# Optimization experiments

Measured on AMD Instinct MI355X. Metric: run time of the kernel, lower is better.

## Reference

```python
import jax, jax.numpy as jnp
import numpy as np

N = 50000
NEG_SLOPE = 0.2


def add_self_loops(edge_index, n):
    loops = jnp.arange(n, dtype=edge_index.dtype)
    return jnp.concatenate([edge_index, jnp.stack([loops, loops])], axis=1)


def gat_layer(x, edge_index, W, a_src, a_dst, b, heads, ch):
    # x: [N, F_in], W: [F_in, heads*ch], a_src/a_dst: [heads, ch], b: [heads*ch]
    n = x.shape[0]
    src, dst = edge_index[0], edge_index[1]
    h = (x @ W).reshape(n, heads, ch)                      # [N, H, C]
    alpha_src = jnp.sum(h * a_src, axis=-1)                # [N, H]
    alpha_dst = jnp.sum(h * a_dst, axis=-1)                # [N, H]
    e = jax.nn.leaky_relu(alpha_src[src] + alpha_dst[dst], NEG_SLOPE)  # [E, H]
    # segment softmax over incoming edges of each destination node
    m = jax.ops.segment_max(e, dst, num_segments=n)        # [N, H]
    ex = jnp.exp(e - m[dst])                               # [E, H]
    denom = jax.ops.segment_sum(ex, dst, num_segments=n)   # [N, H]
    alpha = ex / (denom[dst] + 1e-16)                      # [E, H]
    msg = h[src] * alpha[:, :, None]                       # [E, H, C]
    out = jax.ops.segment_sum(msg, dst, num_segments=n)    # [N, H, C]
    return out.reshape(n, heads * ch) + b


def setup_inputs() -> dict:
    key = jax.random.key(0)
    ks = jax.random.split(key, 12)
    input_dim, hidden_dim, output_dim, heads = 128, 32, 64, 4
    E = 1600000
    x = jax.random.normal(ks[0], (N, input_dim), dtype=jnp.float32)
    edge_index = jax.random.randint(ks[1], (2, E), 0, N, dtype=jnp.int64)
    s1 = 1.0 / np.sqrt(input_dim)
    s2 = 1.0 / np.sqrt(hidden_dim * heads)
    W1 = jax.random.uniform(ks[2], (input_dim, heads * hidden_dim), jnp.float32, -s1, s1)
    a_src1 = jax.random.uniform(ks[3], (heads, hidden_dim), jnp.float32, -s1, s1)
    a_dst1 = jax.random.uniform(ks[4], (heads, hidden_dim), jnp.float32, -s1, s1)
    b1 = jnp.zeros((heads * hidden_dim,), jnp.float32)
    W2 = jax.random.uniform(ks[5], (heads * hidden_dim, output_dim), jnp.float32, -s2, s2)
    a_src2 = jax.random.uniform(ks[6], (1, output_dim), jnp.float32, -s2, s2)
    a_dst2 = jax.random.uniform(ks[7], (1, output_dim), jnp.float32, -s2, s2)
    b2 = jnp.zeros((output_dim,), jnp.float32)
    return {"x": x, "edge_index": edge_index,
            "W1": W1, "a_src1": a_src1, "a_dst1": a_dst1, "b1": b1,
            "W2": W2, "a_src2": a_src2, "a_dst2": a_dst2, "b2": b2}


def reference(x, edge_index, W1, a_src1, a_dst1, b1, W2, a_src2, a_dst2, b2):
    n = x.shape[0]
    ei = add_self_loops(edge_index, n)
    h = gat_layer(x, ei, W1, a_src1, a_dst1, b1, heads=4, ch=32)
    h = jax.nn.relu(h)
    out = gat_layer(h, ei, W2, a_src2, a_dst2, b2, heads=1, ch=64)
    return out
```

## Files before the change

### kernel.cpp

```cpp
#include <hip/hip_runtime.h>
#include <hip/hip_bf16.h>
#include <hip/hip_fp16.h>


#define LRELU_SLOPE 0.2f
#define NBMAX 200
#define NBLK  512
#define BCAP  16384
#define CAPIMG 16384

typedef _Float16 f16x8 __attribute__((ext_vector_type(8)));
typedef float f32x4 __attribute__((ext_vector_type(4)));


__global__ __launch_bounds__(256) void hist_kernel(const int* __restrict__ ei_dst,
                                                   int* __restrict__ hist, int E, int chunk) {
    __shared__ int h[NBMAX];
    int t = threadIdx.x;
    for (int i = t; i < NBMAX; i += 256) h[i] = 0;
    __syncthreads();
    int begin = blockIdx.x * chunk;
    int endE = min(E, begin + chunk);
    for (int e = begin + t; e < endE; e += 256) atomicAdd(&h[ei_dst[e] >> 8], 1);
    __syncthreads();
    for (int i = t; i < NBMAX; i += 256) hist[i * NBLK + blockIdx.x] = h[i];
}

__global__ __launch_bounds__(512) void bucket_scan_kernel(int* __restrict__ hist,
                                                          int* __restrict__ gfill) {
    __shared__ int buf[2][NBLK];
    int b = blockIdx.x, t = threadIdx.x;
    buf[0][t] = hist[b * NBLK + t];
    __syncthreads();
    int pi = 0;
#pragma unroll
    for (int off = 1; off < NBLK; off <<= 1) {
        int v = buf[pi][t];
        if (t >= off) v += buf[pi][t - off];
        buf[pi ^ 1][t] = v;
        __syncthreads();
        pi ^= 1;
    }
    hist[b * NBLK + t] = (t == 0) ? 0 : buf[pi][t - 1];
    if (t == 0) gfill[b] = buf[pi][NBLK - 1];
}

__global__ __launch_bounds__(256) void scatter2_kernel(const int* __restrict__ ei_src,
                                                       const int* __restrict__ ei_dst,
                                                       const int* __restrict__ hist,
                                                       unsigned int* __restrict__ records,
                                                       int E, int chunk) {
    __shared__ int base[NBMAX];
    __shared__ int lcnt[NBMAX];
    int t = threadIdx.x;
    for (int i = t; i < NBMAX; i += 256) {
        base[i] = hist[i * NBLK + blockIdx.x];
        lcnt[i] = 0;
    }
    __syncthreads();
    int begin = blockIdx.x * chunk;
    int endE = min(E, begin + chunk);
    for (int e = begin + t; e < endE; e += 256) {
        int s = ei_src[e], d = ei_dst[e];
        int bkt = d >> 8;
        unsigned int rec = (unsigned int)d | ((unsigned int)s << 16);
        int r = atomicAdd(&lcnt[bkt], 1);
        records[(size_t)bkt * BCAP + base[bkt] + r] = rec;
    }
}

__global__ __launch_bounds__(256) void deg_kernel(const unsigned int* __restrict__ records,
                                                  const int* __restrict__ gfill,
                                                  int* __restrict__ deg, int N) {
    __shared__ int cnt[256];
    int t = threadIdx.x, b = blockIdx.x;
    cnt[t] = 1;
    __syncthreads();
    int c = gfill[b];
    const unsigned int* r = records + (size_t)b * BCAP;
    for (int i = t; i < c; i += 256) atomicAdd(&cnt[r[i] & 255], 1);
    __syncthreads();
    int gi = (b << 8) + t;
    if (gi < N) deg[gi] = cnt[t];
}

__global__ __launch_bounds__(256) void scan_blocksums_kernel(const int* __restrict__ gfill,
                                                             int* __restrict__ bsums,
                                                             int* __restrict__ row_ptr,
                                                             int nblocks, int n, int total) {
    __shared__ int buf[2][256];
    int t = threadIdx.x;
    int v0 = 0;
    if (t < nblocks) v0 = gfill[t] + min(256, n - (t << 8));
    buf[0][t] = v0;
    __syncthreads();
    int pi = 0;
#pragma unroll
    for (int off = 1; off < 256; off <<= 1) {
        int v = buf[pi][t];
        if (t >= off) v += buf[pi][t - off];
        buf[pi ^ 1][t] = v;
        __syncthreads();
        pi ^= 1;
    }
    if (t < nblocks) bsums[t] = (t == 0) ? 0 : buf[pi][t - 1];
    if (t == 0) row_ptr[n] = total;
}

__global__ __launch_bounds__(256) void scan_down_kernel(const int* __restrict__ deg,
                                                        const int* __restrict__ blockSums,
                                                        int* __restrict__ row_ptr, int n) {
    __shared__ int buf[2][256];
    int t = threadIdx.x;
    int i = blockIdx.x * 256 + t;
    int d = (i < n) ? deg[i] : 0;
    buf[0][t] = d;
    __syncthreads();
    int pi = 0;
#pragma unroll
    for (int off = 1; off < 256; off <<= 1) {
        int v = buf[pi][t];
        if (t >= off) v += buf[pi][t - off];
        buf[pi ^ 1][t] = v;
        __syncthreads();
        pi ^= 1;
    }
    if (i < n) row_ptr[i] = blockSums[blockIdx.x] + buf[pi][t] - d;
}

__global__ __launch_bounds__(256) void csr_scatter_kernel(const unsigned int* __restrict__ records,
                                                          const int* __restrict__ gfill,
                                                          const int* __restrict__ row_ptr,
                                                          unsigned short* __restrict__ col,
                                                          int N) {
    __shared__ unsigned short img[CAPIMG];
    __shared__ int lfill[256];
    int t = threadIdx.x, b = blockIdx.x;
    int bBase = b << 8;
    int bEnd = min(bBase + 256, N);
    int rbase = row_ptr[bBase];
    int size = row_ptr[bEnd] - rbase;
    bool lds = (size <= CAPIMG);
    int gi = bBase + t;
    if (gi < bEnd) {
        int rp = row_ptr[gi];
        int local = rp - rbase;
        lfill[t] = local + 1;
        if (lds) img[local] = (unsigned short)gi;
        else col[rp] = (unsigned short)gi;
    }
    __syncthreads();
    int c = gfill[b];
    const unsigned int* r = records + (size_t)b * BCAP;
    for (int i = t; i < c; i += 256) {
        unsigned int rec = r[i];
        int d8 = rec & 255;
        unsigned short s = (unsigned short)(rec >> 16);
        int p = atomicAdd(&lfill[d8], 1);
        if (lds) img[p] = s;
        else col[rbase + p] = s;
    }
    __syncthreads();
    if (lds) {
        for (int i = t; i < size; i += 256) col[rbase + i] = img[i];
    }
}


__global__ __launch_bounds__(256) void gemm1_mfma_kernel(const float* __restrict__ X,
                                                         const float* __restrict__ W,
                                                         __half* __restrict__ outh,
                                                         const float* __restrict__ a_src,
                                                         const float* __restrict__ a_dst,
                                                         float* __restrict__ as_out,
                                                         float* __restrict__ ad_out, int nrows) {
    constexpr int KP = 136;
    __shared__ _Float16 wlds[128 * KP];
    int t = threadIdx.x;
    int wv = t >> 6, lane = t & 63;
    int quad = lane >> 4, m16 = lane & 15;
    for (int i = t; i < 4096; i += 256) {
        int k = i >> 5;
        int n0 = (i & 31) << 2;
        float4 v = *(const float4*)(W + k * 128 + n0);
        wlds[(n0 + 0) * KP + k] = (_Float16)v.x;
        wlds[(n0 + 1) * KP + k] = (_Float16)v.y;
        wlds[(n0 + 2) * KP + k] = (_Float16)v.z;
        wlds[(n0 + 3) * KP + k] = (_Float16)v.w;
    }
    __syncthreads();

    int row = blockIdx.x * 64 + wv * 16 + m16;
    int rowC = min(row, nrows - 1);
    const float* xp = X + (size_t)rowC * 128;

    f32x4 acc[8];
#pragma unroll
    for (int nt = 0; nt < 8; ++nt) acc[nt] = (f32x4)0.f;

    for (int kt = 0; kt < 128; kt += 32) {
        float4 v0 = *(const float4*)(xp + kt + quad * 8);
        float4 v1 = *(const float4*)(xp + kt + quad * 8 + 4);
        f16x8 af;
        af[0] = (_Float16)v0.x; af[1] = (_Float16)v0.y;
        af[2] = (_Float16)v0.z; af[3] = (_Float16)v0.w;
        af[4] = (_Float16)v1.x; af[5] = (_Float16)v1.y;
        af[6] = (_Float16)v1.z; af[7] = (_Float16)v1.w;
#pragma unroll
        for (int nt = 0; nt < 8; ++nt) {
            f16x8 bf = *(const f16x8*)(&wlds[(nt * 16 + m16) * KP + kt + quad * 8]);
            acc[nt] = __builtin_amdgcn_mfma_f32_16x16x32_f16(af, bf, acc[nt], 0, 0, 0);
        }
    }

    float aS[8], aD[8];
#pragma unroll
    for (int nt = 0; nt < 8; ++nt) {
        aS[nt] = a_src[nt * 16 + m16];
        aD[nt] = a_dst[nt * 16 + m16];
    }
    int rowBaseW = blockIdx.x * 64 + wv * 16;
#pragma unroll
    for (int r = 0; r < 4; ++r) {
        int orow = rowBaseW + quad * 4 + r;
        bool ov = orow < nrows;
        if (ov) {
#pragma unroll
            for (int nt = 0; nt < 8; ++nt)
                outh[(size_t)orow * 128 + nt * 16 + m16] = __float2half(acc[nt][r]);
        }
#pragma unroll
        for (int h = 0; h < 4; ++h) {
            float ss = acc[2 * h][r] * aS[2 * h] + acc[2 * h + 1][r] * aS[2 * h + 1];
            float dd = acc[2 * h][r] * aD[2 * h] + acc[2 * h + 1][r] * aD[2 * h + 1];
#pragma unroll
            for (int o = 1; o < 16; o <<= 1) {
                ss += __shfl_xor(ss, o, 64);
                dd += __shfl_xor(dd, o, 64);
            }
            if (ov && m16 == h) {
                as_out[orow * 4 + h] = ss;
                ad_out[orow * 4 + h] = dd;
            }
        }
    }
}


__global__ __launch_bounds__(256) void gemm2_mfma_kernel(const __half* __restrict__ Xh,
                                                         const float* __restrict__ W,
                                                         __half* __restrict__ outh,
                                                         const float* __restrict__ a_src,
                                                         const float* __restrict__ a_dst,
                                                         float* __restrict__ as_out,
                                                         float* __restrict__ ad_out, int nrows) {
    constexpr int KP = 136;
    __shared__ _Float16 wlds[64 * KP];
    int t = threadIdx.x;
    int wv = t >> 6, lane = t & 63;
    int quad = lane >> 4, m16 = lane & 15;
    for (int i = t; i < 2048; i += 256) {
        int k = i >> 4;
        int n0 = (i & 15) << 2;
        float4 v = *(const float4*)(W + k * 64 + n0);
        wlds[(n0 + 0) * KP + k] = (_Float16)v.x;
        wlds[(n0 + 1) * KP + k] = (_Float16)v.y;
        wlds[(n0 + 2) * KP + k] = (_Float16)v.z;
        wlds[(n0 + 3) * KP + k] = (_Float16)v.w;
    }
    __syncthreads();

    int row = blockIdx.x * 64 + wv * 16 + m16;
    int rowC = min(row, nrows - 1);
    const _Float16* xp = (const _Float16*)Xh + (size_t)rowC * 128;

    f32x4 acc[4];
#pragma unroll
    for (int nt = 0; nt < 4; ++nt) acc[nt] = (f32x4)0.f;

    for (int kt = 0; kt < 128; kt += 32) {
        f16x8 af = *(const f16x8*)(xp + kt + quad * 8);
#pragma unroll
        for (int nt = 0; nt < 4; ++nt) {
            f16x8 bf = *(const f16x8*)(&wlds[(nt * 16 + m16) * KP + kt + quad * 8]);
            acc[nt] = __builtin_amdgcn_mfma_f32_16x16x32_f16(af, bf, acc[nt], 0, 0, 0);
        }
    }

    float aS[4], aD[4];
#pragma unroll
    for (int nt = 0; nt < 4; ++nt) {
        aS[nt] = a_src[nt * 16 + m16];
        aD[nt] = a_dst[nt * 16 + m16];
    }
    int rowBaseW = blockIdx.x * 64 + wv * 16;
#pragma unroll
    for (int r = 0; r < 4; ++r) {
        int orow = rowBaseW + quad * 4 + r;
        bool ov = orow < nrows;
        if (ov) {
#pragma unroll
            for (int nt = 0; nt < 4; ++nt)
                outh[(size_t)orow * 64 + nt * 16 + m16] = __float2half(acc[nt][r]);
        }
        float ss = 0.f, dd = 0.f;
#pragma unroll
        for (int nt = 0; nt < 4; ++nt) {
            ss = fmaf(acc[nt][r], aS[nt], ss);
            dd = fmaf(acc[nt][r], aD[nt], dd);
        }
#pragma unroll
        for (int o = 1; o < 16; o <<= 1) {
            ss += __shfl_xor(ss, o, 64);
            dd += __shfl_xor(dd, o, 64);
        }
        if (ov && m16 == 0) {
            as_out[orow] = ss;
            ad_out[orow] = dd;
        }
    }
}


__global__ __launch_bounds__(256) void agg1_kernel(const __half2* __restrict__ h1h,
                                                   const float* __restrict__ asrc,
                                                   const float* __restrict__ adst,
                                                   const int* __restrict__ row_ptr,
                                                   const unsigned short* __restrict__ col,
                                                   const float* __restrict__ b1,
                                                   __half2* __restrict__ out, int n) {
    int wave = threadIdx.x >> 6;
    int lane = threadIdx.x & 63;
    int node = blockIdx.x * 4 + wave;
    if (node >= n) return;
    int head = lane >> 4;
    int hp1 = lane & 3;
    int j16 = lane >> 2;
    float ad1 = adst[node * 4 + hp1];
    int start = row_ptr[node], end = row_ptr[node + 1];
    float accx = 0.f, accy = 0.f, s = 0.f;
    for (int base = start; base < end; base += 64) {
        int idx = base + lane;
        int cnt = min(64, end - base);
        int myS = (idx < end) ? (int)col[idx] : 0;
        float pr[4];
#pragma unroll
        for (int e = 0; e < 4; ++e) {
            int j = e * 16 + j16;
            int srcj = __shfl(myS, j, 64);
            float ev = asrc[srcj * 4 + hp1] + ad1;
            ev = (ev > 0.f) ? ev : LRELU_SLOPE * ev;
            pr[e] = (j < cnt) ? __expf(ev) : 0.f;
        }
#pragma unroll
        for (int e = 0; e < 4; ++e) {
            int ebase = e << 4;
            if (ebase < cnt) {
                float pre = pr[e];
                int rem4 = min(16, ((cnt - ebase) + 3) & ~3);
                for (int jj = 0; jj < rem4; jj += 4) {
                    int j0 = ebase + jj;
                    unsigned s0 = (unsigned)__shfl(myS, j0, 64);
                    unsigned s1 = (unsigned)__shfl(myS, j0 + 1, 64);
                    unsigned s2 = (unsigned)__shfl(myS, j0 + 2, 64);
                    unsigned s3 = (unsigned)__shfl(myS, j0 + 3, 64);
                    float p0 = __shfl(pre, (jj + 0) * 4 + head, 64);
                    float p1 = __shfl(pre, (jj + 1) * 4 + head, 64);
                    float p2 = __shfl(pre, (jj + 2) * 4 + head, 64);
                    float p3 = __shfl(pre, (jj + 3) * 4 + head, 64);
                    float2 f0 = __half22float2(h1h[(s0 << 6) | lane]);
                    float2 f1 = __half22float2(h1h[(s1 << 6) | lane]);
                    float2 f2 = __half22float2(h1h[(s2 << 6) | lane]);
                    float2 f3 = __half22float2(h1h[(s3 << 6) | lane]);
                    accx = fmaf(p0, f0.x, accx);
                    accy = fmaf(p0, f0.y, accy);
                    accx = fmaf(p1, f1.x, accx);
                    accy = fmaf(p1, f1.y, accy);
                    accx = fmaf(p2, f2.x, accx);
                    accy = fmaf(p2, f2.y, accy);
                    accx = fmaf(p3, f3.x, accx);
                    accy = fmaf(p3, f3.y, accy);
                    s += (p0 + p1) + (p2 + p3);
                }
            }
        }
    }
    float inv = 1.f / (s + 1e-16f);
    float2 bb = ((const float2*)b1)[lane];
    float ox = fmaxf(accx * inv + bb.x, 0.f);
    float oy = fmaxf(accy * inv + bb.y, 0.f);
    out[((unsigned)node << 6) | lane] = __floats2half2_rn(ox, oy);
}

__global__ __launch_bounds__(256) void agg2_kernel(const __half2* __restrict__ h2bh,
                                                   const float* __restrict__ asrc,
                                                   const float* __restrict__ adst,
                                                   const int* __restrict__ row_ptr,
                                                   const unsigned short* __restrict__ col,
                                                   const float* __restrict__ b2,
                                                   float* __restrict__ out, int n) {
    int wave = threadIdx.x >> 6;
    int lane = threadIdx.x & 63;
    int node = blockIdx.x * 4 + wave;
    if (node >= n) return;
    int half = lane >> 5;
    int m = lane & 31;
    float ad = adst[node];
    int start = row_ptr[node], end = row_ptr[node + 1];
    float accx = 0.f, accy = 0.f, s = 0.f;
    for (int base = start; base < end; base += 64) {
        int idx = base + lane;
        int cnt = min(64, end - base);
        int myS = (idx < end) ? (int)col[idx] : 0;
        float ev = asrc[myS] + ad;
        ev = (ev > 0.f) ? ev : LRELU_SLOPE * ev;
        float pr = (lane < cnt) ? __expf(ev) : 0.f;
        for (int j = 0; j < cnt; j += 8) {
            int j0 = j + half;
            unsigned s0 = (unsigned)__shfl(myS, j0, 64);
            unsigned s1 = (unsigned)__shfl(myS, j0 + 2, 64);
            unsigned s2 = (unsigned)__shfl(myS, j0 + 4, 64);
            unsigned s3 = (unsigned)__shfl(myS, j0 + 6, 64);
            float p0 = __shfl(pr, j0, 64);
            float p1 = __shfl(pr, j0 + 2, 64);
            float p2 = __shfl(pr, j0 + 4, 64);
            float p3 = __shfl(pr, j0 + 6, 64);
            float2 f0 = __half22float2(h2bh[(s0 << 5) | m]);
            float2 f1 = __half22float2(h2bh[(s1 << 5) | m]);
            float2 f2 = __half22float2(h2bh[(s2 << 5) | m]);
            float2 f3 = __half22float2(h2bh[(s3 << 5) | m]);
            accx = fmaf(p0, f0.x, accx);
            accy = fmaf(p0, f0.y, accy);
            accx = fmaf(p1, f1.x, accx);
            accy = fmaf(p1, f1.y, accy);
            accx = fmaf(p2, f2.x, accx);
            accy = fmaf(p2, f2.y, accy);
            accx = fmaf(p3, f3.x, accx);
            accy = fmaf(p3, f3.y, accy);
            s += (p0 + p1) + (p2 + p3);
        }
    }
    s += __shfl_xor(s, 32, 64);
    accx += __shfl_xor(accx, 32, 64);
    accy += __shfl_xor(accy, 32, 64);
    if (half == 0) {
        float inv = 1.f / (s + 1e-16f);
        float2 bb = ((const float2*)b2)[m];
        float2 o;
        o.x = accx * inv + bb.x;
        o.y = accy * inv + bb.y;
        *(float2*)(out + (size_t)node * 64 + 2 * m) = o;
    }
}


extern "C" void kernel_launch(void* const* d_in, const int* in_sizes, int n_in,
                              void* d_out, int out_size, void* d_ws, size_t ws_size,
                              hipStream_t stream) {
    const float* x      = (const float*)d_in[0];
    const int*   ei     = (const int*)d_in[1];
    const float* W1     = (const float*)d_in[2];
    const float* a_src1 = (const float*)d_in[3];
    const float* a_dst1 = (const float*)d_in[4];
    const float* b1     = (const float*)d_in[5];
    const float* W2     = (const float*)d_in[6];
    const float* a_src2 = (const float*)d_in[7];
    const float* a_dst2 = (const float*)d_in[8];
    const float* b2     = (const float*)d_in[9];
    float* out = (float*)d_out;

    const int N = in_sizes[0] / 128;
    const int E = in_sizes[1] / 2;
    const int total = E + N;
    const int nBuckets = (N + 255) >> 8;

    char* ws = (char*)d_ws;
    size_t off = 0;
    auto alloc = [&](size_t bytes) {
        void* p = ws + off;
        off += (bytes + 255) & ~(size_t)255;
        return p;
    };
    float* regionA = (float*)alloc((size_t)N * 128 * 4);
    __half* h1h   = (__half*)alloc((size_t)N * 128 * 2);
    __half* h2bh  = (__half*)alloc((size_t)N * 64 * 2);
    float* asrc1  = (float*)alloc((size_t)N * 4 * 4);
    float* adst1  = (float*)alloc((size_t)N * 4 * 4);
    float* asrc2  = (float*)alloc((size_t)N * 4);
    float* adst2  = (float*)alloc((size_t)N * 4);
    int*   deg    = (int*)alloc((size_t)N * 4);
    int*   row_ptr= (int*)alloc((size_t)(N + 1) * 4);
    int*   gfill  = (int*)alloc((size_t)nBuckets * 4);
    int*   bsums  = (int*)alloc((size_t)nBuckets * 4);
    unsigned short* col = (unsigned short*)alloc((size_t)total * 2);

    unsigned int* records = (unsigned int*)regionA;
    int* hist = (int*)(regionA + (size_t)NBMAX * BCAP);
    __half* h2in = (__half*)regionA;
    (void)ws_size; (void)n_in; (void)out_size;

    const int* ei_src = ei;
    const int* ei_dst = ei + E;

    const int chunk = (E + NBLK - 1) / NBLK;
    hist_kernel<<<NBLK, 256, 0, stream>>>(ei_dst, hist, E, chunk);
    bucket_scan_kernel<<<nBuckets, NBLK, 0, stream>>>(hist, gfill);
    scatter2_kernel<<<NBLK, 256, 0, stream>>>(ei_src, ei_dst, hist, records, E, chunk);
    deg_kernel<<<nBuckets, 256, 0, stream>>>(records, gfill, deg, N);
    scan_blocksums_kernel<<<1, 256, 0, stream>>>(gfill, bsums, row_ptr, nBuckets, N, total);
    scan_down_kernel<<<nBuckets, 256, 0, stream>>>(deg, bsums, row_ptr, N);
    csr_scatter_kernel<<<nBuckets, 256, 0, stream>>>(records, gfill, row_ptr, col, N);

    gemm1_mfma_kernel<<<(N + 63) / 64, 256, 0, stream>>>(x, W1, h1h, a_src1, a_dst1,
                                                         asrc1, adst1, N);
    agg1_kernel<<<(N + 3) / 4, 256, 0, stream>>>((const __half2*)h1h, asrc1, adst1,
                                                 row_ptr, col, b1, (__half2*)h2in, N);

    gemm2_mfma_kernel<<<(N + 63) / 64, 256, 0, stream>>>(h2in, W2, h2bh, a_src2, a_dst2,
                                                         asrc2, adst2, N);
    agg2_kernel<<<(N + 3) / 4, 256, 0, stream>>>((const __half2*)h2bh, asrc2, adst2,
                                                 row_ptr, col, b2, out, N);
}
```

Measured before the change: 250.7 us.

## Fuse CSR degree/scan/scatter kernels and vectorize aggregation gathers to 16-byte loads

Merges the degree count, per-bucket scan and CSR scatter into one kernel that computes local offsets in shared memory, dropping two launches and the deg array round trip. Both aggregation kernels now have each lane gather 8 fp16 features with one 16-byte load and handle several edges in parallel across lane groups. The partial sums are then reduced across lanes with xor shuffles. This trades more registers and cross-lane reduction work for fewer, wider memory transactions per gathered row.

```diff
diff --git a/kernel.cpp b/kernel.cpp
--- a/kernel.cpp
+++ b/kernel.cpp
@@ -69,21 +69,6 @@
     }
 }
 
-__global__ __launch_bounds__(256) void deg_kernel(const unsigned int* __restrict__ records,
-                                                  const int* __restrict__ gfill,
-                                                  int* __restrict__ deg, int N) {
-    __shared__ int cnt[256];
-    int t = threadIdx.x, b = blockIdx.x;
-    cnt[t] = 1;
-    __syncthreads();
-    int c = gfill[b];
-    const unsigned int* r = records + (size_t)b * BCAP;
-    for (int i = t; i < c; i += 256) atomicAdd(&cnt[r[i] & 255], 1);
-    __syncthreads();
-    int gi = (b << 8) + t;
-    if (gi < N) deg[gi] = cnt[t];
-}
-
 __global__ __launch_bounds__(256) void scan_blocksums_kernel(const int* __restrict__ gfill,
                                                              int* __restrict__ bsums,
                                                              int* __restrict__ row_ptr,
@@ -107,13 +92,26 @@
     if (t == 0) row_ptr[n] = total;
 }
 
-__global__ __launch_bounds__(256) void scan_down_kernel(const int* __restrict__ deg,
-                                                        const int* __restrict__ blockSums,
-                                                        int* __restrict__ row_ptr, int n) {
+__global__ __launch_bounds__(256) void csr_build_kernel(const unsigned int* __restrict__ records,
+                                                        const int* __restrict__ gfill,
+                                                        const int* __restrict__ bsums,
+                                                        int* __restrict__ row_ptr,
+                                                        unsigned short* __restrict__ col,
+                                                        int N) {
+    __shared__ int cnt[256];
     __shared__ int buf[2][256];
-    int t = threadIdx.x;
-    int i = blockIdx.x * 256 + t;
-    int d = (i < n) ? deg[i] : 0;
+    __shared__ unsigned short img[CAPIMG];
+    __shared__ int lfill[256];
+    int t = threadIdx.x, b = blockIdx.x;
+    int gi = (b << 8) + t;
+    bool valid = gi < N;
+    cnt[t] = valid ? 1 : 0;
+    __syncthreads();
+    int c = gfill[b];
+    const unsigned int* r = records + (size_t)b * BCAP;
+    for (int i = t; i < c; i += 256) atomicAdd(&cnt[r[i] & 255], 1);
+    __syncthreads();
+    int d = cnt[t];
     buf[0][t] = d;
     __syncthreads();
     int pi = 0;
@@ -125,33 +123,18 @@
         __syncthreads();
         pi ^= 1;
     }
-    if (i < n) row_ptr[i] = blockSums[blockIdx.x] + buf[pi][t] - d;
-}
-
-__global__ __launch_bounds__(256) void csr_scatter_kernel(const unsigned int* __restrict__ records,
-                                                          const int* __restrict__ gfill,
-                                                          const int* __restrict__ row_ptr,
-                                                          unsigned short* __restrict__ col,
-                                                          int N) {
-    __shared__ unsigned short img[CAPIMG];
-    __shared__ int lfill[256];
-    int t = threadIdx.x, b = blockIdx.x;
-    int bBase = b << 8;
-    int bEnd = min(bBase + 256, N);
-    int rbase = row_ptr[bBase];
-    int size = row_ptr[bEnd] - rbase;
+    int rbase = bsums[b];
+    int nvalid = min(256, N - (b << 8));
+    int size = c + max(nvalid, 0);
     bool lds = (size <= CAPIMG);
-    int gi = bBase + t;
-    if (gi < bEnd) {
-        int rp = row_ptr[gi];
-        int local = rp - rbase;
+    if (valid) {
+        int local = buf[pi][t] - d;
+        row_ptr[gi] = rbase + local;
         lfill[t] = local + 1;
         if (lds) img[local] = (unsigned short)gi;
-        else col[rp] = (unsigned short)gi;
-    }
-    __syncthreads();
-    int c = gfill[b];
-    const unsigned int* r = records + (size_t)b * BCAP;
+        else col[rbase + local] = (unsigned short)gi;
+    }
+    __syncthreads();
     for (int i = t; i < c; i += 256) {
         unsigned int rec = r[i];
         int d8 = rec & 255;
@@ -322,23 +305,29 @@
 }
 
 
-__global__ __launch_bounds__(256) void agg1_kernel(const __half2* __restrict__ h1h,
+__global__ __launch_bounds__(256) void agg1_kernel(const __half* __restrict__ h1h,
                                                    const float* __restrict__ asrc,
                                                    const float* __restrict__ adst,
                                                    const int* __restrict__ row_ptr,
                                                    const unsigned short* __restrict__ col,
                                                    const float* __restrict__ b1,
-                                                   __half2* __restrict__ out, int n) {
+                                                   __half* __restrict__ out, int n) {
     int wave = threadIdx.x >> 6;
     int lane = threadIdx.x & 63;
     int node = blockIdx.x * 4 + wave;
     if (node >= n) return;
-    int head = lane >> 4;
+    int g = lane >> 4;
+    int c16 = lane & 15;
+    int headA = c16 >> 2;
     int hp1 = lane & 3;
     int j16 = lane >> 2;
     float ad1 = adst[node * 4 + hp1];
     int start = row_ptr[node], end = row_ptr[node + 1];
-    float accx = 0.f, accy = 0.f, s = 0.f;
+    float acc[8];
+#pragma unroll
+    for (int k = 0; k < 8; ++k) acc[k] = 0.f;
+    float s = 0.f;
+    const _Float16* hp = (const _Float16*)h1h;
     for (int base = start; base < end; base += 64) {
         int idx = base + lane;
         int cnt = min(64, end - base);
@@ -357,42 +346,44 @@
             int ebase = e << 4;
             if (ebase < cnt) {
                 float pre = pr[e];
-                int rem4 = min(16, ((cnt - ebase) + 3) & ~3);
-                for (int jj = 0; jj < rem4; jj += 4) {
-                    int j0 = ebase + jj;
-                    unsigned s0 = (unsigned)__shfl(myS, j0, 64);
-                    unsigned s1 = (unsigned)__shfl(myS, j0 + 1, 64);
-                    unsigned s2 = (unsigned)__shfl(myS, j0 + 2, 64);
-                    unsigned s3 = (unsigned)__shfl(myS, j0 + 3, 64);
-                    float p0 = __shfl(pre, (jj + 0) * 4 + head, 64);
-                    float p1 = __shfl(pre, (jj + 1) * 4 + head, 64);
-                    float p2 = __shfl(pre, (jj + 2) * 4 + head, 64);
-                    float p3 = __shfl(pre, (jj + 3) * 4 + head, 64);
-                    float2 f0 = __half22float2(h1h[(s0 << 6) | lane]);
-                    float2 f1 = __half22float2(h1h[(s1 << 6) | lane]);
-                    float2 f2 = __half22float2(h1h[(s2 << 6) | lane]);
-                    float2 f3 = __half22float2(h1h[(s3 << 6) | lane]);
-                    accx = fmaf(p0, f0.x, accx);
-                    accy = fmaf(p0, f0.y, accy);
-                    accx = fmaf(p1, f1.x, accx);
-                    accy = fmaf(p1, f1.y, accy);
-                    accx = fmaf(p2, f2.x, accx);
-                    accy = fmaf(p2, f2.y, accy);
-                    accx = fmaf(p3, f3.x, accx);
-                    accy = fmaf(p3, f3.y, accy);
-                    s += (p0 + p1) + (p2 + p3);
+                int lim = min(ebase + 16, cnt);
+                for (int j0 = ebase; j0 < lim; j0 += 4) {
+                    int edge = j0 + g;
+                    unsigned src = (unsigned)__shfl(myS, edge, 64);
+                    float p = __shfl(pre, ((edge & 15) << 2) + headA, 64);
+                    f16x8 hv = *(const f16x8*)(hp + ((size_t)src << 7) + (c16 << 3));
+#pragma unroll
+                    for (int k = 0; k < 8; ++k) acc[k] = fmaf(p, (float)hv[k], acc[k]);
+                    s += p;
                 }
             }
         }
     }
-    float inv = 1.f / (s + 1e-16f);
-    float2 bb = ((const float2*)b1)[lane];
-    float ox = fmaxf(accx * inv + bb.x, 0.f);
-    float oy = fmaxf(accy * inv + bb.y, 0.f);
-    out[((unsigned)node << 6) | lane] = __floats2half2_rn(ox, oy);
-}
-
-__global__ __launch_bounds__(256) void agg2_kernel(const __half2* __restrict__ h2bh,
+    s += __shfl_xor(s, 16, 64);
+    s += __shfl_xor(s, 32, 64);
+#pragma unroll
+    for (int k = 0; k < 8; ++k) {
+        acc[k] += __shfl_xor(acc[k], 16, 64);
+        acc[k] += __shfl_xor(acc[k], 32, 64);
+    }
+    if (g == 0) {
+        float inv = 1.f / (s + 1e-16f);
+        float4 bb0 = ((const float4*)b1)[c16 * 2];
+        float4 bb1 = ((const float4*)b1)[c16 * 2 + 1];
+        f16x8 o;
+        o[0] = (_Float16)fmaxf(acc[0] * inv + bb0.x, 0.f);
+        o[1] = (_Float16)fmaxf(acc[1] * inv + bb0.y, 0.f);
+        o[2] = (_Float16)fmaxf(acc[2] * inv + bb0.z, 0.f);
+        o[3] = (_Float16)fmaxf(acc[3] * inv + bb0.w, 0.f);
+        o[4] = (_Float16)fmaxf(acc[4] * inv + bb1.x, 0.f);
+        o[5] = (_Float16)fmaxf(acc[5] * inv + bb1.y, 0.f);
+        o[6] = (_Float16)fmaxf(acc[6] * inv + bb1.z, 0.f);
+        o[7] = (_Float16)fmaxf(acc[7] * inv + bb1.w, 0.f);
+        *(f16x8*)((_Float16*)out + ((size_t)node << 7) + (c16 << 3)) = o;
+    }
+}
+
+__global__ __launch_bounds__(256) void agg2_kernel(const __half* __restrict__ h2bh,
                                                    const float* __restrict__ asrc,
                                                    const float* __restrict__ adst,
                                                    const int* __restrict__ row_ptr,
@@ -403,11 +394,15 @@
     int lane = threadIdx.x & 63;
     int node = blockIdx.x * 4 + wave;
     if (node >= n) return;
-    int half = lane >> 5;
-    int m = lane & 31;
+    int g = lane >> 3;
+    int c8 = lane & 7;
     float ad = adst[node];
     int start = row_ptr[node], end = row_ptr[node + 1];
-    float accx = 0.f, accy = 0.f, s = 0.f;
+    float acc[8];
+#pragma unroll
+    for (int k = 0; k < 8; ++k) acc[k] = 0.f;
+    float s = 0.f;
+    const _Float16* hp = (const _Float16*)h2bh;
     for (int base = start; base < end; base += 64) {
         int idx = base + lane;
         int cnt = min(64, end - base);
@@ -415,41 +410,41 @@
         float ev = asrc[myS] + ad;
         ev = (ev > 0.f) ? ev : LRELU_SLOPE * ev;
         float pr = (lane < cnt) ? __expf(ev) : 0.f;
-        for (int j = 0; j < cnt; j += 8) {
-            int j0 = j + half;
-            unsigned s0 = (unsigned)__shfl(myS, j0, 64);
-            unsigned s1 = (unsigned)__shfl(myS, j0 + 2, 64);
-            unsigned s2 = (unsigned)__shfl(myS, j0 + 4, 64);
-            unsigned s3 = (unsigned)__shfl(myS, j0 + 6, 64);
-            float p0 = __shfl(pr, j0, 64);
-            float p1 = __shfl(pr, j0 + 2, 64);
-            float p2 = __shfl(pr, j0 + 4, 64);
-            float p3 = __shfl(pr, j0 + 6, 64);
-            float2 f0 = __half22float2(h2bh[(s0 << 5) | m]);
-            float2 f1 = __half22float2(h2bh[(s1 << 5) | m]);
-            float2 f2 = __half22float2(h2bh[(s2 << 5) | m]);
-            float2 f3 = __half22float2(h2bh[(s3 << 5) | m]);
-            accx = fmaf(p0, f0.x, accx);
-            accy = fmaf(p0, f0.y, accy);
-            accx = fmaf(p1, f1.x, accx);
-            accy = fmaf(p1, f1.y, accy);
-            accx = fmaf(p2, f2.x, accx);
-            accy = fmaf(p2, f2.y, accy);
-            accx = fmaf(p3, f3.x, accx);
-            accy = fmaf(p3, f3.y, accy);
-            s += (p0 + p1) + (p2 + p3);
-        }
-    }
+        for (int j0 = 0; j0 < cnt; j0 += 8) {
+            int edge = j0 + g;
+            unsigned src = (unsigned)__shfl(myS, edge, 64);
+            float p = __shfl(pr, edge, 64);
+            f16x8 hv = *(const f16x8*)(hp + ((size_t)src << 6) + (c8 << 3));
+#pragma unroll
+            for (int k = 0; k < 8; ++k) acc[k] = fmaf(p, (float)hv[k], acc[k]);
+            s += p;
+        }
+    }
+    s += __shfl_xor(s, 8, 64);
+    s += __shfl_xor(s, 16, 64);
     s += __shfl_xor(s, 32, 64);
-    accx += __shfl_xor(accx, 32, 64);
-    accy += __shfl_xor(accy, 32, 64);
-    if (half == 0) {
+#pragma unroll
+    for (int k = 0; k < 8; ++k) {
+        acc[k] += __shfl_xor(acc[k], 8, 64);
+        acc[k] += __shfl_xor(acc[k], 16, 64);
+        acc[k] += __shfl_xor(acc[k], 32, 64);
+    }
+    if (g == 0) {
         float inv = 1.f / (s + 1e-16f);
-        float2 bb = ((const float2*)b2)[m];
-        float2 o;
-        o.x = accx * inv + bb.x;
-        o.y = accy * inv + bb.y;
-        *(float2*)(out + (size_t)node * 64 + 2 * m) = o;
+        float4 bb0 = ((const float4*)b2)[c8 * 2];
+        float4 bb1 = ((const float4*)b2)[c8 * 2 + 1];
+        float4 o0, o1;
+        o0.x = acc[0] * inv + bb0.x;
+        o0.y = acc[1] * inv + bb0.y;
+        o0.z = acc[2] * inv + bb0.z;
+        o0.w = acc[3] * inv + bb0.w;
+        o1.x = acc[4] * inv + bb1.x;
+        o1.y = acc[5] * inv + bb1.y;
+        o1.z = acc[6] * inv + bb1.z;
+        o1.w = acc[7] * inv + bb1.w;
+        float* op = out + (size_t)node * 64 + c8 * 8;
+        *(float4*)op = o0;
+        *(float4*)(op + 4) = o1;
     }
 }
 
@@ -488,7 +483,6 @@
     float* adst1  = (float*)alloc((size_t)N * 4 * 4);
     float* asrc2  = (float*)alloc((size_t)N * 4);
     float* adst2  = (float*)alloc((size_t)N * 4);
-    int*   deg    = (int*)alloc((size_t)N * 4);
     int*   row_ptr= (int*)alloc((size_t)(N + 1) * 4);
     int*   gfill  = (int*)alloc((size_t)nBuckets * 4);
     int*   bsums  = (int*)alloc((size_t)nBuckets * 4);
@@ -506,18 +500,16 @@
     hist_kernel<<<NBLK, 256, 0, stream>>>(ei_dst, hist, E, chunk);
     bucket_scan_kernel<<<nBuckets, NBLK, 0, stream>>>(hist, gfill);
     scatter2_kernel<<<NBLK, 256, 0, stream>>>(ei_src, ei_dst, hist, records, E, chunk);
-    deg_kernel<<<nBuckets, 256, 0, stream>>>(records, gfill, deg, N);
     scan_blocksums_kernel<<<1, 256, 0, stream>>>(gfill, bsums, row_ptr, nBuckets, N, total);
-    scan_down_kernel<<<nBuckets, 256, 0, stream>>>(deg, bsums, row_ptr, N);
-    csr_scatter_kernel<<<nBuckets, 256, 0, stream>>>(records, gfill, row_ptr, col, N);
+    csr_build_kernel<<<nBuckets, 256, 0, stream>>>(records, gfill, bsums, row_ptr, col, N);
 
     gemm1_mfma_kernel<<<(N + 63) / 64, 256, 0, stream>>>(x, W1, h1h, a_src1, a_dst1,
                                                          asrc1, adst1, N);
-    agg1_kernel<<<(N + 3) / 4, 256, 0, stream>>>((const __half2*)h1h, asrc1, adst1,
-                                                 row_ptr, col, b1, (__half2*)h2in, N);
+    agg1_kernel<<<(N + 3) / 4, 256, 0, stream>>>(h1h, asrc1, adst1,
+                                                 row_ptr, col, b1, h2in, N);
 
     gemm2_mfma_kernel<<<(N + 63) / 64, 256, 0, stream>>>(h2in, W2, h2bh, a_src2, a_dst2,
                                                          asrc2, adst2, N);
-    agg2_kernel<<<(N + 3) / 4, 256, 0, stream>>>((const __half2*)h2bh, asrc2, adst2,
+    agg2_kernel<<<(N + 3) / 4, 256, 0, stream>>>(h2bh, asrc2, adst2,
                                                  row_ptr, col, b2, out, N);
 }
```

New measurement: 253.3 us. About the same (+1.0%).
